# Performance work log

Measured on AMD Instinct MI355X. Metric: run time of the kernel, lower is better.

The kernel has to match this reference:

```python
import jax, jax.numpy as jnp
import numpy as np

BETA_MIN = 0.1
BETA_MAX = 20.0


def _Beta(t):
    # integral of linear beta schedule
    return BETA_MIN * t + 0.5 * (BETA_MAX - BETA_MIN) * t ** 2


def setup_inputs() -> dict:
    key = jax.random.key(0)
    k1, k2, k3, k4, k5 = jax.random.split(key, 5)
    B, K, D = 4096, 128, 256
    x = jax.random.normal(k1, (B, D), dtype=jnp.float32)
    t = jax.random.uniform(k2, (B,), dtype=jnp.float32)
    centers = jax.random.normal(k3, (K, D), dtype=jnp.float32)
    # keep stds positive and well-conditioned
    stds = 0.5 + 0.5 * jax.random.uniform(k4, (K, D), dtype=jnp.float32)
    # positive mixture weights (original only requires positivity, takes log)
    weights = 0.1 + jax.random.uniform(k5, (K,), dtype=jnp.float32)
    return {"x": x, "t": t, "centers": centers, "stds": stds, "weights": weights}


def reference(x, t, centers, stds, weights):
    ndim = centers.shape[1]

    def log_prob(xx):
        Bt = _Beta(t)[:, None, None]                 # [B,1,1]
        a = jnp.exp(-Bt / 2)
        centers_t = a * centers[None]                # [B,K,D]
        var_t = jnp.exp(-Bt) * stds[None] ** 2 + 1.0 - jnp.exp(-Bt)  # [B,K,D]
        diff = xx[:, None, :] - centers_t            # [B,K,D]
        # NOTE: faithful to source, which uses ndim/2 * sum(log(2*pi*var)) (not 1/2)
        lp = (-(diff ** 2) / (2.0 * var_t)).sum(-1) \
             - (ndim / 2) * jnp.log(2.0 * jnp.pi * var_t).sum(-1)    # [B,K]
        lp = lp + jnp.log(weights)[None, :]
        return jax.scipy.special.logsumexp(lp, axis=1)               # [B]

    grad_log_prob = jax.grad(lambda xx: log_prob(xx).sum())(x)       # [B,D]
    Bt = _Beta(t)[:, None]                                           # [B,1]
    return -jnp.sqrt(1.0 - jnp.exp(-Bt)) * grad_log_prob
```

## Files before the change

### kernel.cpp

```cpp
#include <hip/hip_runtime.h>
#include <math.h>


constexpr int Kc = 128;
constexpr int Dc = 256;
constexpr int G  = 4;

typedef float f2 __attribute__((ext_vector_type(2)));
typedef float f4 __attribute__((ext_vector_type(4)));

static __device__ __forceinline__ f2 fma2(f2 a, f2 b, f2 c) {
    return __builtin_elementwise_fma(a, b, c);
}
static __device__ __forceinline__ f2 splat2(float s) { return (f2){s, s}; }

__global__ void prep_kernel(const float* __restrict__ centers,
                            const float* __restrict__ stds,
                            float* __restrict__ CA8, f2* __restrict__ P2) {
    int idx = blockIdx.x * blockDim.x + threadIdx.x;
    if (idx >= Kc * Dc) return;
    int k = idx >> 8;
    int d = idx & (Dc - 1);
    float c = centers[idx];
    float s = stds[idx];
    float A = s * s - 1.0f;
    int o = (d >> 2) * (Kc * 8) + k * 8 + (d & 3);
    CA8[o]     = c;
    CA8[o + 4] = A;
    P2[idx] = (f2){c, A};
}

__global__ __launch_bounds__(256, 6) void score_kernel(
    const float* __restrict__ x, const float* __restrict__ t,
    const float* __restrict__ weights,
    const float* __restrict__ CA8, const f2* __restrict__ P2,
    float* __restrict__ out)
{
    const int b0  = blockIdx.x * G;
    const int tid = threadIdx.x;

    __shared__ __align__(16) float xT[Dc][G];
    __shared__ float part1[G][2][Kc];
    __shared__ float partL[G][2][Kc];
    __shared__ __align__(16) float peT[Kc][G];
    __shared__ float wmax[G][2];
    __shared__ float wsum[G][2];

    float e[G], na[G], sg[G];
    #pragma unroll
    for (int g = 0; g < G; ++g) {
        float tt = t[b0 + g];
        float Bt = fmaf(9.95f * tt, tt, 0.1f * tt);
        float ee = __expf(-Bt);
        e[g]  = ee;
        na[g] = -sqrtf(ee);
        sg[g] = sqrtf(1.0f - ee);
    }
    f2 e2[2]  = {{e[0], e[1]}, {e[2], e[3]}};
    f2 na2[2] = {{na[0], na[1]}, {na[2], na[3]}};
    const f2 one2 = {1.0f, 1.0f};

    #pragma unroll
    for (int g = 0; g < G; ++g)
        xT[tid][g] = x[(b0 + g) * Dc + tid];
    __syncthreads();

    const int kk    = tid & (Kc - 1);
    const int half  = tid >> 7;
    const int dbase = half * (Dc / 2);

    const f4* xTv = (const f4*)(&xT[0][0]);

    f2 acc1[2] = {{0.f, 0.f}, {0.f, 0.f}};
    float accL[G] = {0.f, 0.f, 0.f, 0.f};

    for (int grp = 0; grp < 8; ++grp) {
        f2 prod[2] = {{1.f, 1.f}, {1.f, 1.f}};
        #pragma unroll
        for (int q = 0; q < 4; ++q) {
            const int d0 = dbase + (grp * 4 + q) * 4;
            const float* base = CA8 + ((size_t)(d0 >> 2) * Kc + kk) * 8;
            f4 c4 = *(const f4*)base;
            f4 A4 = *(const f4*)(base + 4);
            f4 xv0 = xTv[d0 + 0];
            f4 xv1 = xTv[d0 + 1];
            f4 xv2 = xTv[d0 + 2];
            f4 xv3 = xTv[d0 + 3];
            #pragma unroll
            for (int p = 0; p < 2; ++p) {
                f2 ep = e2[p], nap = na2[p];
                f2 x0 = {xv0[2*p], xv0[2*p+1]};
                f2 x1 = {xv1[2*p], xv1[2*p+1]};
                f2 x2 = {xv2[2*p], xv2[2*p+1]};
                f2 x3 = {xv3[2*p], xv3[2*p+1]};
                f2 v0 = fma2(ep, splat2(A4[0]), one2);
                f2 v1 = fma2(ep, splat2(A4[1]), one2);
                f2 v2 = fma2(ep, splat2(A4[2]), one2);
                f2 v3 = fma2(ep, splat2(A4[3]), one2);
                f2 f0 = fma2(nap, splat2(c4[0]), x0);
                f2 f1 = fma2(nap, splat2(c4[1]), x1);
                f2 f2_ = fma2(nap, splat2(c4[2]), x2);
                f2 f3 = fma2(nap, splat2(c4[3]), x3);
                f2 s0 = f0 * f0, s1 = f1 * f1, s2 = f2_ * f2_, s3 = f3 * f3;
                f2 d01 = v0 * v1, d23 = v2 * v3;
                f2 n01 = fma2(s1, v0, s0 * v1);
                f2 n23 = fma2(s3, v2, s2 * v3);
                f2 den = d01 * d23;
                f2 num = fma2(n23, d01, n01 * d23);
                f2 r = {__builtin_amdgcn_rcpf(den[0]),
                        __builtin_amdgcn_rcpf(den[1])};
                acc1[p] = fma2(num, r, acc1[p]);
                prod[p] = prod[p] * den;
            }
        }
        accL[0] += __log2f(prod[0][0]);
        accL[1] += __log2f(prod[0][1]);
        accL[2] += __log2f(prod[1][0]);
        accL[3] += __log2f(prod[1][1]);
    }
    #pragma unroll
    for (int p = 0; p < 2; ++p) {
        part1[2*p  ][half][kk] = acc1[p][0];
        part1[2*p+1][half][kk] = acc1[p][1];
    }
    #pragma unroll
    for (int g = 0; g < G; ++g)
        partL[g][half][kk] = accL[g];
    __syncthreads();

    float lpv[G];
    if (tid < Kc) {
        float lw = __logf(weights[tid]);
        #pragma unroll
        for (int g = 0; g < G; ++g) {
            float S1 = part1[g][0][tid] + part1[g][1][tid];
            float S2 = partL[g][0][tid] + partL[g][1][tid];
            lpv[g] = fmaf(-0.5f, S1, fmaf(-88.72283911167299f, S2, lw));
            float m = lpv[g];
            #pragma unroll
            for (int off = 32; off > 0; off >>= 1)
                m = fmaxf(m, __shfl_xor(m, off, 64));
            if ((tid & 63) == 0) wmax[g][tid >> 6] = m;
        }
    }
    __syncthreads();
    if (tid < Kc) {
        #pragma unroll
        for (int g = 0; g < G; ++g) {
            float m  = fmaxf(wmax[g][0], wmax[g][1]);
            float pe = __expf(lpv[g] - m);
            peT[tid][g] = pe;
            float s = pe;
            #pragma unroll
            for (int off = 32; off > 0; off >>= 1)
                s += __shfl_xor(s, off, 64);
            if ((tid & 63) == 0) wsum[g][tid >> 6] = s;
        }
    }
    __syncthreads();

    f4 xvv = xTv[tid];
    f2 xp[2] = {{xvv[0], xvv[1]}, {xvv[2], xvv[3]}};
    f2 O[2] = {{0.f, 0.f}, {0.f, 0.f}};
    const f4* peTv = (const f4*)(&peT[0][0]);
    const f2* pp = P2 + tid;

    for (int kq = 0; kq < 32; ++kq) {
        const int k0 = kq * 4;
        f2 ca0 = pp[(k0 + 0) * Dc];
        f2 ca1 = pp[(k0 + 1) * Dc];
        f2 ca2 = pp[(k0 + 2) * Dc];
        f2 ca3 = pp[(k0 + 3) * Dc];
        f4 p0 = peTv[k0 + 0];
        f4 p1 = peTv[k0 + 1];
        f4 p2 = peTv[k0 + 2];
        f4 p3 = peTv[k0 + 3];
        #pragma unroll
        for (int p = 0; p < 2; ++p) {
            f2 ep = e2[p], nap = na2[p];
            f2 v0 = fma2(ep, splat2(ca0[1]), one2);
            f2 v1 = fma2(ep, splat2(ca1[1]), one2);
            f2 v2 = fma2(ep, splat2(ca2[1]), one2);
            f2 v3 = fma2(ep, splat2(ca3[1]), one2);
            f2 f0 = fma2(nap, splat2(ca0[0]), xp[p]);
            f2 f1 = fma2(nap, splat2(ca1[0]), xp[p]);
            f2 f2_ = fma2(nap, splat2(ca2[0]), xp[p]);
            f2 f3 = fma2(nap, splat2(ca3[0]), xp[p]);
            f2 u0 = (f2){p0[2*p], p0[2*p+1]} * f0;
            f2 u1 = (f2){p1[2*p], p1[2*p+1]} * f1;
            f2 u2 = (f2){p2[2*p], p2[2*p+1]} * f2_;
            f2 u3 = (f2){p3[2*p], p3[2*p+1]} * f3;
            f2 d01 = v0 * v1, d23 = v2 * v3;
            f2 n01 = fma2(u1, v0, u0 * v1);
            f2 n23 = fma2(u3, v2, u2 * v3);
            f2 den = d01 * d23;
            f2 num = fma2(n23, d01, n01 * d23);
            f2 r = {__builtin_amdgcn_rcpf(den[0]),
                    __builtin_amdgcn_rcpf(den[1])};
            O[p] = fma2(num, r, O[p]);
        }
    }

    #pragma unroll
    for (int p = 0; p < 2; ++p) {
        #pragma unroll
        for (int j = 0; j < 2; ++j) {
            int g = 2 * p + j;
            float Z = wsum[g][0] + wsum[g][1];
            out[(b0 + g) * Dc + tid] = sg[g] * __builtin_amdgcn_rcpf(Z) * O[p][j];
        }
    }
}

extern "C" void kernel_launch(void* const* d_in, const int* in_sizes, int n_in,
                              void* d_out, int out_size, void* d_ws, size_t ws_size,
                              hipStream_t stream) {
    const float* x       = (const float*)d_in[0];
    const float* t       = (const float*)d_in[1];
    const float* centers = (const float*)d_in[2];
    const float* stds    = (const float*)d_in[3];
    const float* weights = (const float*)d_in[4];
    float* outp = (float*)d_out;

    float* CA8 = (float*)d_ws;
    f2*    P2  = (f2*)(CA8 + Kc * Dc * 2);

    const int B = in_sizes[1];

    prep_kernel<<<(Kc * Dc + 255) / 256, 256, 0, stream>>>(centers, stds, CA8, P2);
    score_kernel<<<B / G, 256, 0, stream>>>(x, t, weights, CA8, P2, outp);
}
```

Baseline: 102.1 us.

## Skip negligible mixture components in gradient pass and merge reciprocals over 8 dims

The first pass now merges two 4-dim groups into one fraction, so it issues one reciprocal per 8 dimensions instead of one per 4. After the softmax, each block builds a compacted list of components whose log-prob lies within 25 of the max for any of its 4 rows. The gradient pass then loops only over those components, in pairs. This removes work for components whose weight is effectively zero. The trade-offs are a lower occupancy hint, more denominator multiplications that could overflow or underflow, and a small error from the dropped components.

Result: slower. 106.8 us (+4.6%).

```diff
diff --git a/kernel.cpp b/kernel.cpp
--- a/kernel.cpp
+++ b/kernel.cpp
@@ -13,6 +13,9 @@
     return __builtin_elementwise_fma(a, b, c);
 }
 static __device__ __forceinline__ f2 splat2(float s) { return (f2){s, s}; }
+static __device__ __forceinline__ f2 rcp2(f2 a) {
+    return (f2){__builtin_amdgcn_rcpf(a[0]), __builtin_amdgcn_rcpf(a[1])};
+}
 
 __global__ void prep_kernel(const float* __restrict__ centers,
                             const float* __restrict__ stds,
@@ -30,7 +33,7 @@
     P2[idx] = (f2){c, A};
 }
 
-__global__ __launch_bounds__(256, 6) void score_kernel(
+__global__ __launch_bounds__(256, 4) void score_kernel(
     const float* __restrict__ x, const float* __restrict__ t,
     const float* __restrict__ weights,
     const float* __restrict__ CA8, const f2* __restrict__ P2,
@@ -39,12 +42,15 @@
     const int b0  = blockIdx.x * G;
     const int tid = threadIdx.x;
 
-    __shared__ __align__(16) float xT[Dc][G];
+    __shared__ __align__(16) f4 xT[Dc];
     __shared__ float part1[G][2][Kc];
     __shared__ float partL[G][2][Kc];
-    __shared__ __align__(16) float peT[Kc][G];
+    __shared__ __align__(16) f4 peT[Kc];
     __shared__ float wmax[G][2];
     __shared__ float wsum[G][2];
+    __shared__ int wcnt[2];
+    __shared__ int klist[Kc];
+    __shared__ int nk_s;
 
     float e[G], na[G], sg[G];
     #pragma unroll
@@ -60,57 +66,68 @@
     f2 na2[2] = {{na[0], na[1]}, {na[2], na[3]}};
     const f2 one2 = {1.0f, 1.0f};
 
-    #pragma unroll
-    for (int g = 0; g < G; ++g)
-        xT[tid][g] = x[(b0 + g) * Dc + tid];
+    {
+        f4 xv;
+        #pragma unroll
+        for (int g = 0; g < G; ++g) xv[g] = x[(b0 + g) * Dc + tid];
+        xT[tid] = xv;
+    }
     __syncthreads();
 
     const int kk    = tid & (Kc - 1);
     const int half  = tid >> 7;
     const int dbase = half * (Dc / 2);
 
-    const f4* xTv = (const f4*)(&xT[0][0]);
+    const f4* xTv = (const f4*)(&xT[0]);
 
     f2 acc1[2] = {{0.f, 0.f}, {0.f, 0.f}};
     float accL[G] = {0.f, 0.f, 0.f, 0.f};
 
-    for (int grp = 0; grp < 8; ++grp) {
+    for (int u4 = 0; u4 < 4; ++u4) {
         f2 prod[2] = {{1.f, 1.f}, {1.f, 1.f}};
         #pragma unroll
-        for (int q = 0; q < 4; ++q) {
-            const int d0 = dbase + (grp * 4 + q) * 4;
-            const float* base = CA8 + ((size_t)(d0 >> 2) * Kc + kk) * 8;
-            f4 c4 = *(const f4*)base;
-            f4 A4 = *(const f4*)(base + 4);
-            f4 xv0 = xTv[d0 + 0];
-            f4 xv1 = xTv[d0 + 1];
-            f4 xv2 = xTv[d0 + 2];
-            f4 xv3 = xTv[d0 + 3];
+        for (int uu = 0; uu < 4; ++uu) {
+            const int d0 = dbase + (u4 * 4 + uu) * 8;
+            f2 num8[2], den8[2];
             #pragma unroll
-            for (int p = 0; p < 2; ++p) {
-                f2 ep = e2[p], nap = na2[p];
-                f2 x0 = {xv0[2*p], xv0[2*p+1]};
-                f2 x1 = {xv1[2*p], xv1[2*p+1]};
-                f2 x2 = {xv2[2*p], xv2[2*p+1]};
-                f2 x3 = {xv3[2*p], xv3[2*p+1]};
-                f2 v0 = fma2(ep, splat2(A4[0]), one2);
-                f2 v1 = fma2(ep, splat2(A4[1]), one2);
-                f2 v2 = fma2(ep, splat2(A4[2]), one2);
-                f2 v3 = fma2(ep, splat2(A4[3]), one2);
-                f2 f0 = fma2(nap, splat2(c4[0]), x0);
-                f2 f1 = fma2(nap, splat2(c4[1]), x1);
-                f2 f2_ = fma2(nap, splat2(c4[2]), x2);
-                f2 f3 = fma2(nap, splat2(c4[3]), x3);
-                f2 s0 = f0 * f0, s1 = f1 * f1, s2 = f2_ * f2_, s3 = f3 * f3;
-                f2 d01 = v0 * v1, d23 = v2 * v3;
-                f2 n01 = fma2(s1, v0, s0 * v1);
-                f2 n23 = fma2(s3, v2, s2 * v3);
-                f2 den = d01 * d23;
-                f2 num = fma2(n23, d01, n01 * d23);
-                f2 r = {__builtin_amdgcn_rcpf(den[0]),
-                        __builtin_amdgcn_rcpf(den[1])};
-                acc1[p] = fma2(num, r, acc1[p]);
-                prod[p] = prod[p] * den;
+            for (int h = 0; h < 2; ++h) {
+                const int dq = d0 + h * 4;
+                const float* base = CA8 + ((size_t)(dq >> 2) * Kc + kk) * 8;
+                f4 c4 = *(const f4*)base;
+                f4 A4 = *(const f4*)(base + 4);
+                f4 xv0 = xTv[dq + 0];
+                f4 xv1 = xTv[dq + 1];
+                f4 xv2 = xTv[dq + 2];
+                f4 xv3 = xTv[dq + 3];
+                #pragma unroll
+                for (int p = 0; p < 2; ++p) {
+                    f2 ep = e2[p], nap = na2[p];
+                    f2 x0 = {xv0[2*p], xv0[2*p+1]};
+                    f2 x1 = {xv1[2*p], xv1[2*p+1]};
+                    f2 x2 = {xv2[2*p], xv2[2*p+1]};
+                    f2 x3 = {xv3[2*p], xv3[2*p+1]};
+                    f2 v0 = fma2(ep, splat2(A4[0]), one2);
+                    f2 v1 = fma2(ep, splat2(A4[1]), one2);
+                    f2 v2 = fma2(ep, splat2(A4[2]), one2);
+                    f2 v3 = fma2(ep, splat2(A4[3]), one2);
+                    f2 f0 = fma2(nap, splat2(c4[0]), x0);
+                    f2 f1 = fma2(nap, splat2(c4[1]), x1);
+                    f2 f2_ = fma2(nap, splat2(c4[2]), x2);
+                    f2 f3 = fma2(nap, splat2(c4[3]), x3);
+                    f2 s0 = f0 * f0, s1 = f1 * f1, s2 = f2_ * f2_, s3 = f3 * f3;
+                    f2 d01 = v0 * v1, d23 = v2 * v3;
+                    f2 n01 = fma2(s1, v0, s0 * v1);
+                    f2 n23 = fma2(s3, v2, s2 * v3);
+                    f2 den = d01 * d23;
+                    f2 num = fma2(n23, d01, n01 * d23);
+                    if (h == 0) { num8[p] = num; den8[p] = den; }
+                    else {
+                        f2 dU = den8[p] * den;
+                        f2 nU = fma2(num, den8[p], num8[p] * den);
+                        acc1[p] = fma2(nU, rcp2(dU), acc1[p]);
+                        prod[p] = prod[p] * dU;
+                    }
+                }
             }
         }
         accL[0] += __log2f(prod[0][0]);
@@ -129,6 +146,8 @@
     __syncthreads();
 
     float lpv[G];
+    bool flag = false;
+    int myoff = 0;
     if (tid < Kc) {
         float lw = __logf(weights[tid]);
         #pragma unroll
@@ -145,59 +164,63 @@
     }
     __syncthreads();
     if (tid < Kc) {
+        f4 pe4;
         #pragma unroll
         for (int g = 0; g < G; ++g) {
             float m  = fmaxf(wmax[g][0], wmax[g][1]);
             float pe = __expf(lpv[g] - m);
-            peT[tid][g] = pe;
+            pe4[g] = pe;
+            flag |= (lpv[g] >= m - 25.0f);
             float s = pe;
             #pragma unroll
             for (int off = 32; off > 0; off >>= 1)
                 s += __shfl_xor(s, off, 64);
             if ((tid & 63) == 0) wsum[g][tid >> 6] = s;
         }
-    }
-    __syncthreads();
-
-    f4 xvv = xTv[tid];
-    f2 xp[2] = {{xvv[0], xvv[1]}, {xvv[2], xvv[3]}};
+        peT[tid] = pe4;
+        unsigned long long msk = __ballot(flag);
+        int lane = tid & 63;
+        if (lane == 0) wcnt[tid >> 6] = __popcll(msk);
+        myoff = __popcll(msk & ((1ull << lane) - 1ull));
+    }
+    __syncthreads();
+    if (tid < Kc) {
+        if (flag) {
+            int basei = (tid >= 64) ? wcnt[0] : 0;
+            klist[basei + myoff] = tid;
+        }
+        if (tid == 0) nk_s = wcnt[0] + wcnt[1];
+    }
+    __syncthreads();
+
+    const int nk = nk_s;
+    f4 xv = xT[tid];
+    f2 xp[2] = {{xv[0], xv[1]}, {xv[2], xv[3]}};
     f2 O[2] = {{0.f, 0.f}, {0.f, 0.f}};
-    const f4* peTv = (const f4*)(&peT[0][0]);
     const f2* pp = P2 + tid;
 
-    for (int kq = 0; kq < 32; ++kq) {
-        const int k0 = kq * 4;
-        f2 ca0 = pp[(k0 + 0) * Dc];
-        f2 ca1 = pp[(k0 + 1) * Dc];
-        f2 ca2 = pp[(k0 + 2) * Dc];
-        f2 ca3 = pp[(k0 + 3) * Dc];
-        f4 p0 = peTv[k0 + 0];
-        f4 p1 = peTv[k0 + 1];
-        f4 p2 = peTv[k0 + 2];
-        f4 p3 = peTv[k0 + 3];
+    for (int i = 0; i < nk; i += 2) {
+        int ka = klist[i];
+        bool hasb = (i + 1 < nk);
+        int kb = hasb ? klist[i + 1] : ka;
+        float sb = hasb ? 1.0f : 0.0f;
+        f2 caA = pp[ka * Dc];
+        f2 caB = pp[kb * Dc];
+        f4 peA = peT[ka];
+        f4 peB = peT[kb];
+        peB *= sb;
         #pragma unroll
         for (int p = 0; p < 2; ++p) {
             f2 ep = e2[p], nap = na2[p];
-            f2 v0 = fma2(ep, splat2(ca0[1]), one2);
-            f2 v1 = fma2(ep, splat2(ca1[1]), one2);
-            f2 v2 = fma2(ep, splat2(ca2[1]), one2);
-            f2 v3 = fma2(ep, splat2(ca3[1]), one2);
-            f2 f0 = fma2(nap, splat2(ca0[0]), xp[p]);
-            f2 f1 = fma2(nap, splat2(ca1[0]), xp[p]);
-            f2 f2_ = fma2(nap, splat2(ca2[0]), xp[p]);
-            f2 f3 = fma2(nap, splat2(ca3[0]), xp[p]);
-            f2 u0 = (f2){p0[2*p], p0[2*p+1]} * f0;
-            f2 u1 = (f2){p1[2*p], p1[2*p+1]} * f1;
-            f2 u2 = (f2){p2[2*p], p2[2*p+1]} * f2_;
-            f2 u3 = (f2){p3[2*p], p3[2*p+1]} * f3;
-            f2 d01 = v0 * v1, d23 = v2 * v3;
-            f2 n01 = fma2(u1, v0, u0 * v1);
-            f2 n23 = fma2(u3, v2, u2 * v3);
-            f2 den = d01 * d23;
-            f2 num = fma2(n23, d01, n01 * d23);
-            f2 r = {__builtin_amdgcn_rcpf(den[0]),
-                    __builtin_amdgcn_rcpf(den[1])};
-            O[p] = fma2(num, r, O[p]);
+            f2 vA = fma2(ep, splat2(caA[1]), one2);
+            f2 vB = fma2(ep, splat2(caB[1]), one2);
+            f2 fA = fma2(nap, splat2(caA[0]), xp[p]);
+            f2 fB = fma2(nap, splat2(caB[0]), xp[p]);
+            f2 uA = (f2){peA[2*p], peA[2*p+1]} * fA;
+            f2 uB = (f2){peB[2*p], peB[2*p+1]} * fB;
+            f2 den = vA * vB;
+            f2 num = fma2(uB, vA, uA * vB);
+            O[p] = fma2(num, rcp2(den), O[p]);
         }
     }
 
```

## Split score kernel work across 512-thread blocks with shared-memory partial reductions

Applied to the files above, without the earlier changes.

Doubles the block size to 512 threads. The log-prob phase now splits the D dimension into quarters instead of halves, and the gradient phase splits the K loop into two halves. The halves are combined through a new shared-memory buffer and an extra barrier. The aim is to shorten each thread's serial loop and expose more parallelism per block, at the cost of extra synchronisation, more shared memory and tighter register limits from the new launch bounds. Some leftover dead temporaries remain in the inner loop.

Result: slower. 104.5 us (+2.4%).

```diff
diff --git a/kernel.cpp b/kernel.cpp
--- a/kernel.cpp
+++ b/kernel.cpp
@@ -13,6 +13,9 @@
     return __builtin_elementwise_fma(a, b, c);
 }
 static __device__ __forceinline__ f2 splat2(float s) { return (f2){s, s}; }
+static __device__ __forceinline__ f2 rcp2(f2 a) {
+    return (f2){__builtin_amdgcn_rcpf(a[0]), __builtin_amdgcn_rcpf(a[1])};
+}
 
 __global__ void prep_kernel(const float* __restrict__ centers,
                             const float* __restrict__ stds,
@@ -30,7 +33,7 @@
     P2[idx] = (f2){c, A};
 }
 
-__global__ __launch_bounds__(256, 6) void score_kernel(
+__global__ __launch_bounds__(512, 8) void score_kernel(
     const float* __restrict__ x, const float* __restrict__ t,
     const float* __restrict__ weights,
     const float* __restrict__ CA8, const f2* __restrict__ P2,
@@ -39,10 +42,11 @@
     const int b0  = blockIdx.x * G;
     const int tid = threadIdx.x;
 
-    __shared__ __align__(16) float xT[Dc][G];
-    __shared__ float part1[G][2][Kc];
-    __shared__ float partL[G][2][Kc];
-    __shared__ __align__(16) float peT[Kc][G];
+    __shared__ __align__(16) f4 xT[Dc];
+    __shared__ float part1[G][4][Kc];
+    __shared__ float partL[G][4][Kc];
+    __shared__ __align__(16) f4 peT[Kc];
+    __shared__ __align__(16) f4 Opart[Dc];
     __shared__ float wmax[G][2];
     __shared__ float wsum[G][2];
 
@@ -60,21 +64,24 @@
     f2 na2[2] = {{na[0], na[1]}, {na[2], na[3]}};
     const f2 one2 = {1.0f, 1.0f};
 
-    #pragma unroll
-    for (int g = 0; g < G; ++g)
-        xT[tid][g] = x[(b0 + g) * Dc + tid];
+    if (tid < Dc) {
+        f4 xv;
+        #pragma unroll
+        for (int g = 0; g < G; ++g) xv[g] = x[(b0 + g) * Dc + tid];
+        xT[tid] = xv;
+    }
     __syncthreads();
 
     const int kk    = tid & (Kc - 1);
-    const int half  = tid >> 7;
-    const int dbase = half * (Dc / 2);
-
-    const f4* xTv = (const f4*)(&xT[0][0]);
+    const int qtr   = tid >> 7;
+    const int dbase = qtr * (Dc / 4);
+
+    const f4* xTv = (const f4*)(&xT[0]);
 
     f2 acc1[2] = {{0.f, 0.f}, {0.f, 0.f}};
     float accL[G] = {0.f, 0.f, 0.f, 0.f};
 
-    for (int grp = 0; grp < 8; ++grp) {
+    for (int grp = 0; grp < 4; ++grp) {
         f2 prod[2] = {{1.f, 1.f}, {1.f, 1.f}};
         #pragma unroll
         for (int q = 0; q < 4; ++q) {
@@ -107,9 +114,7 @@
                 f2 n23 = fma2(s3, v2, s2 * v3);
                 f2 den = d01 * d23;
                 f2 num = fma2(n23, d01, n01 * d23);
-                f2 r = {__builtin_amdgcn_rcpf(den[0]),
-                        __builtin_amdgcn_rcpf(den[1])};
-                acc1[p] = fma2(num, r, acc1[p]);
+                acc1[p] = fma2(num, rcp2(den), acc1[p]);
                 prod[p] = prod[p] * den;
             }
         }
@@ -120,12 +125,12 @@
     }
     #pragma unroll
     for (int p = 0; p < 2; ++p) {
-        part1[2*p  ][half][kk] = acc1[p][0];
-        part1[2*p+1][half][kk] = acc1[p][1];
+        part1[2*p  ][qtr][kk] = acc1[p][0];
+        part1[2*p+1][qtr][kk] = acc1[p][1];
     }
     #pragma unroll
     for (int g = 0; g < G; ++g)
-        partL[g][half][kk] = accL[g];
+        partL[g][qtr][kk] = accL[g];
     __syncthreads();
 
     float lpv[G];
@@ -133,8 +138,10 @@
         float lw = __logf(weights[tid]);
         #pragma unroll
         for (int g = 0; g < G; ++g) {
-            float S1 = part1[g][0][tid] + part1[g][1][tid];
-            float S2 = partL[g][0][tid] + partL[g][1][tid];
+            float S1 = (part1[g][0][tid] + part1[g][1][tid])
+                     + (part1[g][2][tid] + part1[g][3][tid]);
+            float S2 = (partL[g][0][tid] + partL[g][1][tid])
+                     + (partL[g][2][tid] + partL[g][3][tid]);
             lpv[g] = fmaf(-0.5f, S1, fmaf(-88.72283911167299f, S2, lw));
             float m = lpv[g];
             #pragma unroll
@@ -145,36 +152,39 @@
     }
     __syncthreads();
     if (tid < Kc) {
+        f4 pe4;
         #pragma unroll
         for (int g = 0; g < G; ++g) {
             float m  = fmaxf(wmax[g][0], wmax[g][1]);
             float pe = __expf(lpv[g] - m);
-            peT[tid][g] = pe;
+            pe4[g] = pe;
             float s = pe;
             #pragma unroll
             for (int off = 32; off > 0; off >>= 1)
                 s += __shfl_xor(s, off, 64);
             if ((tid & 63) == 0) wsum[g][tid >> 6] = s;
         }
-    }
-    __syncthreads();
-
-    f4 xvv = xTv[tid];
-    f2 xp[2] = {{xvv[0], xvv[1]}, {xvv[2], xvv[3]}};
+        peT[tid] = pe4;
+    }
+    __syncthreads();
+
+    const int dd = tid & (Dc - 1);
+    const int kh = tid >> 8;
+
+    f4 xv = xT[dd];
+    f2 xp[2] = {{xv[0], xv[1]}, {xv[2], xv[3]}};
     f2 O[2] = {{0.f, 0.f}, {0.f, 0.f}};
-    const f4* peTv = (const f4*)(&peT[0][0]);
-    const f2* pp = P2 + tid;
-
-    for (int kq = 0; kq < 32; ++kq) {
+    const f4* peTv = (const f4*)(&peT[0]);
+    const f2* pp = P2 + dd;
+
+    for (int kq = kh * 16; kq < kh * 16 + 16; ++kq) {
         const int k0 = kq * 4;
         f2 ca0 = pp[(k0 + 0) * Dc];
         f2 ca1 = pp[(k0 + 1) * Dc];
         f2 ca2 = pp[(k0 + 2) * Dc];
         f2 ca3 = pp[(k0 + 3) * Dc];
-        f4 p0 = peTv[k0 + 0];
-        f4 p1 = peTv[k0 + 1];
-        f4 p2 = peTv[k0 + 2];
-        f4 p3 = peTv[k0 + 3];
+        f4 pa = peTv[(k0 >> 1) + 0];
+        f4 pb = peTv[(k0 >> 1) + 1];
         #pragma unroll
         for (int p = 0; p < 2; ++p) {
             f2 ep = e2[p], nap = na2[p];
@@ -186,28 +196,48 @@
             f2 f1 = fma2(nap, splat2(ca1[0]), xp[p]);
             f2 f2_ = fma2(nap, splat2(ca2[0]), xp[p]);
             f2 f3 = fma2(nap, splat2(ca3[0]), xp[p]);
-            f2 u0 = (f2){p0[2*p], p0[2*p+1]} * f0;
-            f2 u1 = (f2){p1[2*p], p1[2*p+1]} * f1;
-            f2 u2 = (f2){p2[2*p], p2[2*p+1]} * f2_;
-            f2 u3 = (f2){p3[2*p], p3[2*p+1]} * f3;
+            f2 u0 = (f2){pa[2*p], pa[2*p+1]} * f0;
+            f2 u1 = (f2){pa[2*p], pa[2*p+1]};
+            u1 = (f2){pa[2*p], pa[2*p+1]};
+            u1 = (f2){pb[0], pb[0]};
+            f2 w0 = {pa[2*p], pa[2*p+1]};
+            f2 w1 = {pa[2*p], pa[2*p+1]};
+            (void)u1; (void)w1;
+            f2 q0 = {pa[2*p], pa[2*p+1]};
+            (void)q0; (void)w0; (void)u0;
+            f4 peA = peT[k0 + 0];
+            f4 peB = peT[k0 + 1];
+            f4 peC = peT[k0 + 2];
+            f4 peD = peT[k0 + 3];
+            f2 uu0 = (f2){peA[2*p], peA[2*p+1]} * f0;
+            f2 uu1 = (f2){peB[2*p], peB[2*p+1]} * f1;
+            f2 uu2 = (f2){peC[2*p], peC[2*p+1]} * f2_;
+            f2 uu3 = (f2){peD[2*p], peD[2*p+1]} * f3;
             f2 d01 = v0 * v1, d23 = v2 * v3;
-            f2 n01 = fma2(u1, v0, u0 * v1);
-            f2 n23 = fma2(u3, v2, u2 * v3);
+            f2 n01 = fma2(uu1, v0, uu0 * v1);
+            f2 n23 = fma2(uu3, v2, uu2 * v3);
             f2 den = d01 * d23;
             f2 num = fma2(n23, d01, n01 * d23);
-            f2 r = {__builtin_amdgcn_rcpf(den[0]),
-                    __builtin_amdgcn_rcpf(den[1])};
-            O[p] = fma2(num, r, O[p]);
-        }
-    }
-
-    #pragma unroll
-    for (int p = 0; p < 2; ++p) {
-        #pragma unroll
-        for (int j = 0; j < 2; ++j) {
-            int g = 2 * p + j;
-            float Z = wsum[g][0] + wsum[g][1];
-            out[(b0 + g) * Dc + tid] = sg[g] * __builtin_amdgcn_rcpf(Z) * O[p][j];
+            O[p] = fma2(num, rcp2(den), O[p]);
+        }
+    }
+
+    if (kh == 1) {
+        Opart[dd] = (f4){O[0][0], O[0][1], O[1][0], O[1][1]};
+    }
+    __syncthreads();
+
+    if (tid < Dc) {
+        f4 Ou = Opart[tid];
+        #pragma unroll
+        for (int p = 0; p < 2; ++p) {
+            #pragma unroll
+            for (int j = 0; j < 2; ++j) {
+                int g = 2 * p + j;
+                float Z = wsum[g][0] + wsum[g][1];
+                float Osum = O[p][j] + Ou[2 * p + j];
+                out[(b0 + g) * Dc + tid] = sg[g] * __builtin_amdgcn_rcpf(Z) * Osum;
+            }
         }
     }
 }
@@ -228,5 +258,5 @@
     const int B = in_sizes[1];
 
     prep_kernel<<<(Kc * Dc + 255) / 256, 256, 0, stream>>>(centers, stds, CA8, P2);
-    score_kernel<<<B / G, 256, 0, stream>>>(x, t, weights, CA8, P2, outp);
-}
+    score_kernel<<<B / G, 512, 0, stream>>>(x, t, weights, CA8, P2, outp);
+}
```
